# Kernel optimization log

Measured on AMD Instinct MI355X. Metric: run time of the kernel, lower is better.

Reference implementation:

```python
import jax, jax.numpy as jnp
import numpy as np

DIM = 256   # model dim (forced by gate Linear(32,4): d = 32 = DIM//H)
H = 8       # heads (hard-coded by mask.repeat(1,8,1,1))
D = DIM // H
B = 256     # batch
NS = 100    # skeleton tokens (sub-block size)
NQ = 64     # query tokens
N = NS + NQ # 164
NE = 4      # experts
HID = 50    # expert hidden
LN_EPS = 1e-5


def setup_inputs() -> dict:
    key = jax.random.key(0)
    ks = jax.random.split(key, 12)
    s = 0.02
    return {
        "x": jax.random.normal(ks[0], (B, N, DIM), jnp.float32),
        "mask": jax.random.randint(ks[1], (B, N), 0, 2).astype(bool),
        "w_qk_s": jax.random.normal(ks[2], (DIM, 2 * DIM), jnp.float32) * s,
        "w_qk_q": jax.random.normal(ks[3], (DIM, 2 * DIM), jnp.float32) * s,
        "w_v": jax.random.normal(ks[4], (DIM, DIM), jnp.float32) * s,
        "w_gate": jax.random.normal(ks[5], (D, NE), jnp.float32) * s,
        "b_gate": jnp.zeros((NE,), jnp.float32),
        "ln_gamma": jnp.ones((NE,), jnp.float32),
        "ln_beta": jnp.zeros((NE,), jnp.float32),
        "w1": jax.random.normal(ks[6], (NE, NS, HID), jnp.float32) * s,
        "b1": jnp.zeros((NE, HID), jnp.float32),
        "w2": jax.random.normal(ks[7], (NE, HID, NS), jnp.float32) * s,
        "b2": jnp.zeros((NE, NS), jnp.float32),
        "w_out": jax.random.normal(ks[8], (DIM, DIM), jnp.float32) * s,
        "b_out": jnp.zeros((DIM,), jnp.float32),
    }


def reference(x, mask, w_qk_s, w_qk_q, w_v, w_gate, b_gate, ln_gamma, ln_beta,
              w1, b1, w2, b2, w_out, b_out):
    b, n, dim = x.shape
    scale = dim ** -0.5  # scale_with_head=False -> dim**-0.5

    def to_heads(t):  # (b, m, H*D) -> (b, H, m, D)
        return t.reshape(b, -1, H, D).transpose(0, 2, 1, 3)

    # separate qk projections for skeleton (first 100) vs query (last 64) tokens
    q_s, k_s = jnp.split(x[:, :NS] @ w_qk_s, 2, axis=-1)
    q_q, k_q = jnp.split(x[:, NS:] @ w_qk_q, 2, axis=-1)
    q = jnp.concatenate([to_heads(q_s), to_heads(q_q)], axis=2)  # (b,H,N,D)
    k = jnp.concatenate([to_heads(k_s), to_heads(k_q)], axis=2)
    v = to_heads(x @ w_v)

    # gates: RAW reshape of x (b,n,H*D) -> (b,H,n,D) (memory reinterpretation,
    # as in torch x.reshape), detached, sliced to first 100 'rows'
    gx = jax.lax.stop_gradient(x).reshape(b, H, n, D)[:, :, :NS, :]
    g = gx @ w_gate + b_gate                              # (b,H,100,4)
    mu = g.mean(-1, keepdims=True)
    var = g.var(-1, keepdims=True)
    g = (g - mu) / jnp.sqrt(var + LN_EPS) * ln_gamma + ln_beta
    gates = jax.nn.softmax(g, axis=-1)                    # (b,H,100,4)

    dots = jnp.einsum('bhid,bhjd->bhij', q, k) * scale    # (b,H,N,N)
    mask_value = -jnp.finfo(dots.dtype).max
    dots = jnp.where(mask[:, None, None, :], mask_value, dots)

    # soft-MoE over the 100x100 sub-block (experts applied along key axis)
    attn_q = dots[:, :, :NS, :NS]                         # (b,H,100,100)
    h1 = jax.nn.relu(jnp.einsum('bhij,ejk->bheik', jax.nn.relu(attn_q), w1)
                     + b1[:, None, :])                    # (b,H,4,100,50)
    eo = jax.nn.relu(jnp.einsum('bheik,ekj->bheij', h1, w2)
                     + b2[:, None, :])                    # (b,H,4,100,100)
    moes = jnp.einsum('bheij,bhie->bhij', eo, gates)      # (b,H,100,100)

    dots = dots.at[:, :, :NS, :NS].add(moes)
    attn = jax.nn.softmax(dots, axis=-1)
    out = jnp.einsum('bhij,bhjd->bhid', attn, v)          # (b,H,N,D)
    out = out.transpose(0, 2, 1, 3).reshape(b, n, dim)
    return out @ w_out + b_out
```

## Files before the change

### kernel.cpp

```cpp
#include <hip/hip_runtime.h>

typedef __bf16 bf16x8 __attribute__((ext_vector_type(8)));
typedef __bf16 bf16x4 __attribute__((ext_vector_type(4)));
typedef float  f32x4  __attribute__((ext_vector_type(4)));

__device__ __forceinline__ bf16x8 ldb8(const __bf16* p) {
    return *reinterpret_cast<const bf16x8*>(p);
}
__device__ __forceinline__ bf16x8 zero8() {
    bf16x8 z;
    #pragma unroll
    for (int i = 0; i < 8; i++) z[i] = (__bf16)0.f;
    return z;
}
__device__ __forceinline__ __bf16 ldw(const void* p, int i, int m) {
    return m ? (__bf16)((const float*)p)[i] : ((const __bf16*)p)[i];
}
__device__ __forceinline__ bf16x8 ldx8(const void* p, size_t ei, int m) {
    if (m) {
        const float* f = (const float*)p + ei;
        f32x4 a = *reinterpret_cast<const f32x4*>(f);
        f32x4 b = *reinterpret_cast<const f32x4*>(f + 4);
        bf16x8 r;
        #pragma unroll
        for (int u = 0; u < 4; u++) { r[u] = (__bf16)a[u]; r[4 + u] = (__bf16)b[u]; }
        return r;
    }
    return ldb8((const __bf16*)p + ei);
}

__global__ __launch_bounds__(256) void detect_kernel(
    const void* x, const void* mask, int* modes, int* maskws)
{
    __shared__ int v32bad, v16bad, sbad;
    const int t = threadIdx.x, bid = blockIdx.x;
    if (t == 0) { v32bad = 0; v16bad = 0; sbad = 0; }
    __syncthreads();
    const unsigned int* mw = (const unsigned int*)mask;
    int b32 = 0, b16 = 0;
    for (int i = t; i < 10496; i += 256) {
        unsigned int w = mw[i];
        if (!(w == 0u || w == 1u || w == 0x3F800000u)) b32++;
        unsigned int h0 = w & 0xFFFFu, h1 = w >> 16;
        if (!(h0 == 0u || h0 == 1u || h0 == 0x3F80u)) b16++;
        if (!(h1 == 0u || h1 == 1u || h1 == 0x3F80u)) b16++;
    }
    if (b32) atomicAdd(&v32bad, b32);
    if (b16) atomicAdd(&v16bad, b16);
    if (bid == 0) {
        const unsigned int* xw = (const unsigned int*)x;
        int bad = 0;
        for (int i = t; i < 2048; i += 256) {
            unsigned int w = xw[i];
            unsigned int el = (w >> 7) & 0xFF, eh = (w >> 23) & 0xFF;
            if (el >= 0x94 || el == 0xFF) bad++;
            if (eh >= 0x94 || eh == 0xFF) bad++;
        }
        if (bad) atomicAdd(&sbad, bad);
    }
    __syncthreads();
    const int mmode = (v32bad == 0) ? 0 : ((v16bad == 0) ? 2 : 1);
    if (bid == 0 && t == 0) { modes[0] = (sbad > 64) ? 1 : 0; modes[1] = mmode; }
    const int lo = bid * 656, hi = lo + 656;
    for (int i = lo + t; i < hi; i += 256) {
        int val;
        if (mmode == 0)      val = (((const int*)mask)[i] != 0);
        else if (mmode == 2) val = (((const unsigned short*)mask)[i] != 0);
        else                 val = (((const unsigned char*)mask)[i] != 0);
        maskws[i] = val;
    }
}

__global__ __launch_bounds__(256) void prep_kernel(
    const void* wqks, const void* wqkq, const void* wv, const void* w1,
    const void* w2, const void* wout, const void* wg, const void* bg,
    const void* lng, const void* lnb, const void* b1, const void* b2,
    const void* bout, const int* __restrict__ modes,
    __bf16* __restrict__ Wts, __bf16* __restrict__ Wtq,
    __bf16* __restrict__ w1t, __bf16* __restrict__ w2t,
    __bf16* __restrict__ wot, __bf16* __restrict__ wsm)
{
    const int m = modes[0];
    int i = blockIdx.x * 256 + threadIdx.x;
    if (i < 196608) {
        int n = i >> 8, k = i & 255;
        __bf16 vs, vq;
        if (n < 512) { vs = ldw(wqks, k * 512 + n, m); vq = ldw(wqkq, k * 512 + n, m); }
        else         { vs = ldw(wv, k * 256 + (n - 512), m); vq = vs; }
        Wts[i] = vs; Wtq[i] = vq;
        return;
    }
    i -= 196608;
    if (i < 32768) {
        int e = i >> 13, r = i & 8191, n = r >> 7, k = r & 127;
        w1t[i] = (n < 50 && k < 100) ? ldw(w1, (e * 100 + k) * 50 + n, m) : (__bf16)0.f;
        return;
    }
    i -= 32768;
    if (i < 28672) {
        int e = i / 7168, r = i % 7168, n = r >> 6, k = r & 63;
        w2t[i] = (n < 100 && k < 50) ? ldw(w2, (e * 50 + k) * 100 + n, m) : (__bf16)0.f;
        return;
    }
    i -= 28672;
    if (i < 65536) {
        int n = i >> 8, k = i & 255;
        wot[i] = ldw(wout, k * 256 + n, m);
        return;
    }
    i -= 65536;
    if (i < 996) {
        __bf16 v;
        if (i < 128)      v = ldw(wg, i, m);
        else if (i < 132) v = ldw(bg, i - 128, m);
        else if (i < 136) v = ldw(lng, i - 132, m);
        else if (i < 140) v = ldw(lnb, i - 136, m);
        else if (i < 340) v = ldw(b1, i - 140, m);
        else if (i < 740) v = ldw(b2, i - 340, m);
        else              v = ldw(bout, i - 740, m);
        wsm[i] = v;
    }
}

__global__ __launch_bounds__(256, 2) void qkv_kernel(
    const void* __restrict__ x, const __bf16* __restrict__ Wts,
    const __bf16* __restrict__ Wtq, const __bf16* __restrict__ wsm,
    const int* __restrict__ modes,
    __bf16* __restrict__ q, __bf16* __restrict__ k, __bf16* __restrict__ vt,
    float* __restrict__ gates)
{
    __shared__ __bf16 xs[32][264];
    __shared__ float wgf[128];
    __shared__ float gcst[12];
    const int m = modes[0];
    const int b = blockIdx.y;
    const int mt = blockIdx.x >> 1;
    const int half = blockIdx.x & 1;
    const __bf16* Wt = (mt < 4) ? Wts : Wtq;
    const int rbase = (mt < 4) ? mt * 32 : 100 + (mt - 4) * 32;
    const int tid = threadIdx.x;

    if (tid < 128) wgf[tid] = (float)wsm[tid];
    if (tid < 12)  gcst[tid] = (float)wsm[128 + tid];
    for (int c = tid; c < 1024; c += 256) {
        int row = c >> 5, part = c & 31;
        bf16x8 val = ldx8(x, ((size_t)b * 164 + rbase + row) * 256 + part * 8, m);
        *reinterpret_cast<bf16x8*>(&xs[row][part * 8]) = val;
    }
    __syncthreads();

    if (half == 0) {
        int jg = rbase * 8 + tid;
        int h = jg / 164;
        int j = jg - h * 164;
        if (j < 100) {
            const __bf16* xp = &xs[tid >> 3][(tid & 7) * 32];
            float g[4] = {gcst[0], gcst[1], gcst[2], gcst[3]};
            #pragma unroll
            for (int p = 0; p < 4; p++) {
                bf16x8 xv = ldb8(xp + p * 8);
                #pragma unroll
                for (int u = 0; u < 8; u++) {
                    float f = (float)xv[u];
                    #pragma unroll
                    for (int e = 0; e < 4; e++) g[e] += f * wgf[(p * 8 + u) * 4 + e];
                }
            }
            float mu = 0.25f * (g[0] + g[1] + g[2] + g[3]);
            float var = 0.25f * ((g[0]-mu)*(g[0]-mu) + (g[1]-mu)*(g[1]-mu) +
                                 (g[2]-mu)*(g[2]-mu) + (g[3]-mu)*(g[3]-mu));
            float is = rsqrtf(var + 1e-5f);
            float mx = -3.0e38f;
            #pragma unroll
            for (int e = 0; e < 4; e++) {
                g[e] = (g[e] - mu) * is * gcst[4 + e] + gcst[8 + e];
                mx = fmaxf(mx, g[e]);
            }
            float s = 0.f;
            #pragma unroll
            for (int e = 0; e < 4; e++) { g[e] = __expf(g[e] - mx); s += g[e]; }
            float inv = 1.f / s;
            float4 gv = make_float4(g[0]*inv, g[1]*inv, g[2]*inv, g[3]*inv);
            *reinterpret_cast<float4*>(&gates[((size_t)(b * 8 + h) * 100 + j) * 4]) = gv;
        }
    }

    const int w = tid >> 6, l = tid & 63, lr = l & 15, lc = l >> 4;
    f32x4 acc[2][6];
    #pragma unroll
    for (int ms = 0; ms < 2; ms++)
        #pragma unroll
        for (int nt = 0; nt < 6; nt++) acc[ms][nt] = (f32x4){0.f, 0.f, 0.f, 0.f};

    #pragma unroll
    for (int kt = 0; kt < 8; kt++) {
        bf16x8 a0 = ldb8(&xs[lr][kt * 32 + lc * 8]);
        bf16x8 a1 = ldb8(&xs[16 + lr][kt * 32 + lc * 8]);
        #pragma unroll
        for (int nt = 0; nt < 6; nt++) {
            bf16x8 bb = ldb8(Wt + (size_t)(half * 384 + w * 96 + nt * 16 + lr) * 256 + kt * 32 + lc * 8);
            acc[0][nt] = __builtin_amdgcn_mfma_f32_16x16x32_bf16(a0, bb, acc[0][nt], 0, 0, 0);
            acc[1][nt] = __builtin_amdgcn_mfma_f32_16x16x32_bf16(a1, bb, acc[1][nt], 0, 0, 0);
        }
    }
    #pragma unroll
    for (int ms = 0; ms < 2; ms++) {
        #pragma unroll
        for (int nt = 0; nt < 6; nt++) {
            int c = half * 384 + w * 96 + nt * 16 + lr;
            int i0 = rbase + ms * 16 + lc * 4;
            if (c < 512) {
                __bf16* dst; int ch;
                if (c < 256) { dst = q; ch = c; }
                else         { dst = k; ch = c - 256; }
                int hh = ch >> 5, d = ch & 31;
                #pragma unroll
                for (int r = 0; r < 4; r++) {
                    int i = i0 + r;
                    if (mt >= 4 || i < 100)
                        dst[(((size_t)b * 8 + hh) * 164 + i) * 32 + d] = (__bf16)acc[ms][nt][r];
                }
            } else {
                int ch = c - 512, hh = ch >> 5, d = ch & 31;
                if (mt >= 4 || i0 < 100) {
                    bf16x4 pv;
                    #pragma unroll
                    for (int r = 0; r < 4; r++) pv[r] = (__bf16)acc[ms][nt][r];
                    *reinterpret_cast<bf16x4*>(&vt[((size_t)(b * 8 + hh) * 32 + d) * 176 + i0]) = pv;
                }
            }
        }
    }
}

__global__ __launch_bounds__(256, 4) void attn_kernel(
    const __bf16* __restrict__ qg, const __bf16* __restrict__ kg,
    const __bf16* __restrict__ vtg, const float* __restrict__ gatesg,
    const int* __restrict__ maskg, const __bf16* __restrict__ w1t,
    const __bf16* __restrict__ w2t, const __bf16* __restrict__ wsm,
    __bf16* __restrict__ ohg)
{
    __shared__ __align__(16) __bf16 lds[20352];
    const int RS_OFF = 7040;
    const int P_OFF  = 7040;

    const __bf16* b1g = wsm + 140;
    const __bf16* b2g = wsm + 340;
    const int bh = blockIdx.x, rt = blockIdx.y, b = bh >> 3, tid = threadIdx.x;
    const int w = tid >> 6, l = tid & 63, lr = l & 15, lc = l >> 4;
    const int m0 = w * 16;

    const __bf16* kbase = kg + (size_t)bh * 164 * 32;
    for (int c = tid; c < 704; c += 256) {
        int row = c >> 2, part = c & 3;
        bf16x8 val = (row < 164) ? ldb8(kbase + row * 32 + part * 8) : zero8();
        *reinterpret_cast<bf16x8*>(&lds[row * 40 + part * 8]) = val;
    }
    unsigned mbits = 0;
    #pragma unroll
    for (int nt = 0; nt < 11; nt++) {
        int j = nt * 16 + lr;
        int bad = (j < 164) ? maskg[b * 164 + j] : 1;
        mbits |= (bad ? 1u : 0u) << nt;
    }
    int qrow = rt * 64 + m0 + lr; if (qrow > 163) qrow = 163;
    bf16x8 afq = ldb8(qg + ((size_t)bh * 164 + qrow) * 32 + lc * 8);
    __syncthreads();

    f32x4 raw[12];
    #pragma unroll
    for (int nt = 0; nt < 11; nt++) {
        bf16x8 bf = ldb8(&lds[(nt * 16 + lr) * 40 + lc * 8]);
        f32x4 acc = {0.f, 0.f, 0.f, 0.f};
        acc = __builtin_amdgcn_mfma_f32_16x16x32_bf16(afq, bf, acc, 0, 0, 0);
        bool bad = (mbits >> nt) & 1;
        #pragma unroll
        for (int r = 0; r < 4; r++)
            raw[nt][r] = bad ? -1e30f : acc[r] * 0.0625f;
    }
    #pragma unroll
    for (int r = 0; r < 4; r++) raw[11][r] = -1e30f;

    if (rt < 2) {
        #pragma unroll
        for (int nt = 0; nt < 8; nt++) {
            int j = nt * 16 + lr;
            #pragma unroll
            for (int r = 0; r < 4; r++) {
                float v = raw[nt][r];
                v = (j >= 100 || v < 0.f) ? 0.f : v;
                lds[RS_OFF + (m0 + lc * 4 + r) * 136 + j] = (__bf16)v;
            }
        }
    }
    __syncthreads();

    if (rt < 2) {
        const int gi0 = rt * 64 + m0 + lc * 4;
        float4 gv[4];
        #pragma unroll
        for (int r = 0; r < 4; r++) {
            int gi = gi0 + r;
            gv[r] = (gi < 100)
                ? *reinterpret_cast<const float4*>(&gatesg[((size_t)bh * 100 + gi) * 4])
                : make_float4(0.f, 0.f, 0.f, 0.f);
        }
        bf16x8 sa[4];
        #pragma unroll
        for (int kt = 0; kt < 4; kt++)
            sa[kt] = ldb8(&lds[RS_OFF + (m0 + lr) * 136 + kt * 32 + lc * 8]);
        #pragma unroll
        for (int e = 0; e < 4; e++) {
            const int HO = (e & 1) ? 15744 : 0;
            #pragma unroll
            for (int nt = 0; nt < 4; nt++) {
                f32x4 acc = {0.f, 0.f, 0.f, 0.f};
                #pragma unroll
                for (int kt = 0; kt < 4; kt++) {
                    bf16x8 bb = ldb8(w1t + (size_t)(e * 64 + nt * 16 + lr) * 128 + kt * 32 + lc * 8);
                    acc = __builtin_amdgcn_mfma_f32_16x16x32_bf16(sa[kt], bb, acc, 0, 0, 0);
                }
                int n = nt * 16 + lr;
                float bias = (n < 50) ? (float)b1g[e * 50 + n] : 0.f;
                #pragma unroll
                for (int r = 0; r < 4; r++) {
                    float v = acc[r] + bias;
                    if (v < 0.f) v = 0.f;
                    lds[HO + (m0 + lc * 4 + r) * 72 + n] = (__bf16)v;
                }
            }
            bf16x8 ha0 = ldb8(&lds[HO + (m0 + lr) * 72 + lc * 8]);
            bf16x8 ha1 = ldb8(&lds[HO + (m0 + lr) * 72 + 32 + lc * 8]);
            #pragma unroll
            for (int nt = 0; nt < 7; nt++) {
                f32x4 acc = {0.f, 0.f, 0.f, 0.f};
                bf16x8 bb0 = ldb8(w2t + (size_t)(e * 112 + nt * 16 + lr) * 64 + lc * 8);
                acc = __builtin_amdgcn_mfma_f32_16x16x32_bf16(ha0, bb0, acc, 0, 0, 0);
                bf16x8 bb1 = ldb8(w2t + (size_t)(e * 112 + nt * 16 + lr) * 64 + 32 + lc * 8);
                acc = __builtin_amdgcn_mfma_f32_16x16x32_bf16(ha1, bb1, acc, 0, 0, 0);
                int n = nt * 16 + lr;
                float bias = (n < 100) ? (float)b2g[e * 100 + n] : 0.f;
                #pragma unroll
                for (int r = 0; r < 4; r++) {
                    float v = acc[r] + bias;
                    if (v < 0.f) v = 0.f;
                    float ge = (e == 0) ? gv[r].x : (e == 1) ? gv[r].y
                             : (e == 2) ? gv[r].z : gv[r].w;
                    raw[nt][r] += v * ge;
                }
            }
        }
    }
    __syncthreads();

    const __bf16* vtb = vtg + (size_t)bh * 32 * 176;
    int off0, off1, off2;
    bf16x8 vv0, vv1, vv2;
    {
        int c = tid;
        int row = c / 22, j0 = (c - row * 22) * 8;
        off0 = row * 200 + j0;
        if (j0 < 168) {
            vv0 = ldb8(vtb + row * 176 + j0);
            if (j0 == 160) { vv0[4] = (__bf16)0.f; vv0[5] = (__bf16)0.f; vv0[6] = (__bf16)0.f; vv0[7] = (__bf16)0.f; }
        } else vv0 = zero8();
    }
    {
        int c = tid + 256;
        int row = c / 22, j0 = (c - row * 22) * 8;
        off1 = row * 200 + j0;
        if (j0 < 168) {
            vv1 = ldb8(vtb + row * 176 + j0);
            if (j0 == 160) { vv1[4] = (__bf16)0.f; vv1[5] = (__bf16)0.f; vv1[6] = (__bf16)0.f; vv1[7] = (__bf16)0.f; }
        } else vv1 = zero8();
    }
    if (tid < 192) {
        int c = tid + 512;
        int row = c / 22, j0 = (c - row * 22) * 8;
        off2 = row * 200 + j0;
        if (j0 < 168) {
            vv2 = ldb8(vtb + row * 176 + j0);
            if (j0 == 160) { vv2[4] = (__bf16)0.f; vv2[5] = (__bf16)0.f; vv2[6] = (__bf16)0.f; vv2[7] = (__bf16)0.f; }
        } else vv2 = zero8();
    }

    #pragma unroll
    for (int r = 0; r < 4; r++) {
        float x0 = fmaxf(raw[0][r], raw[1][r]);
        float x1 = fmaxf(raw[2][r], raw[3][r]);
        float x2 = fmaxf(raw[4][r], raw[5][r]);
        float x3 = fmaxf(raw[6][r], raw[7][r]);
        float x4 = fmaxf(raw[8][r], raw[9][r]);
        float x5 = fmaxf(raw[10][r], raw[11][r]);
        float m2 = fmaxf(fmaxf(fmaxf(x0, x1), fmaxf(x2, x3)), fmaxf(x4, x5));
        m2 = fmaxf(m2, __shfl_xor(m2, 1, 64));
        m2 = fmaxf(m2, __shfl_xor(m2, 2, 64));
        m2 = fmaxf(m2, __shfl_xor(m2, 4, 64));
        m2 = fmaxf(m2, __shfl_xor(m2, 8, 64));
        #pragma unroll
        for (int nt = 0; nt < 12; nt++) raw[nt][r] = __expf(raw[nt][r] - m2);
        float s0 = (raw[0][r] + raw[1][r]) + (raw[2][r] + raw[3][r]);
        float s1 = (raw[4][r] + raw[5][r]) + (raw[6][r] + raw[7][r]);
        float s2t = (raw[8][r] + raw[9][r]) + (raw[10][r] + raw[11][r]);
        float s2 = (s0 + s1) + s2t;
        s2 += __shfl_xor(s2, 1, 64);
        s2 += __shfl_xor(s2, 2, 64);
        s2 += __shfl_xor(s2, 4, 64);
        s2 += __shfl_xor(s2, 8, 64);
        float inv = (s2 > 0.f) ? 1.f / s2 : 0.f;
        #pragma unroll
        for (int nt = 0; nt < 12; nt++)
            lds[P_OFF + (m0 + lc * 4 + r) * 200 + nt * 16 + lr] = (__bf16)(raw[nt][r] * inv);
    }

    *reinterpret_cast<bf16x8*>(&lds[off0]) = vv0;
    *reinterpret_cast<bf16x8*>(&lds[off1]) = vv1;
    if (tid < 192) *reinterpret_cast<bf16x8*>(&lds[off2]) = vv2;
    __syncthreads();

    int gi = rt * 64 + m0 + lr;
    #pragma unroll
    for (int nt = 0; nt < 2; nt++) {
        f32x4 acc = {0.f, 0.f, 0.f, 0.f};
        #pragma unroll
        for (int kt = 0; kt < 6; kt++) {
            bf16x8 va = ldb8(&lds[(nt * 16 + lr) * 200 + kt * 32 + lc * 8]);
            bf16x8 pb = ldb8(&lds[P_OFF + (m0 + lr) * 200 + kt * 32 + lc * 8]);
            acc = __builtin_amdgcn_mfma_f32_16x16x32_bf16(va, pb, acc, 0, 0, 0);
        }
        if (gi < 164) {
            bf16x4 ov;
            #pragma unroll
            for (int r = 0; r < 4; r++) ov[r] = (__bf16)acc[r];
            *reinterpret_cast<bf16x4*>(&ohg[((size_t)bh * 164 + gi) * 32 + nt * 16 + lc * 4]) = ov;
        }
    }
}

__global__ __launch_bounds__(256) void outproj_kernel(
    const __bf16* __restrict__ oh, const __bf16* __restrict__ wot,
    const __bf16* __restrict__ wsm, float* __restrict__ out)
{
    const __bf16* bout = wsm + 740;
    const int b = blockIdx.y;
    const int mt = blockIdx.x >> 2;
    const int ntile = blockIdx.x & 3;
    const int tid = threadIdx.x;
    const int w = tid >> 6, l = tid & 63, lr = l & 15, lc = l >> 4;
    int row = mt * 64 + w * 16 + lr; if (row > 163) row = 163;
    f32x4 acc[4];
    #pragma unroll
    for (int nt = 0; nt < 4; nt++) acc[nt] = (f32x4){0.f, 0.f, 0.f, 0.f};
    #pragma unroll
    for (int kt = 0; kt < 8; kt++) {
        bf16x8 a = ldb8(oh + (((size_t)b * 8 + kt) * 164 + row) * 32 + lc * 8);
        #pragma unroll
        for (int nt = 0; nt < 4; nt++) {
            bf16x8 bb = ldb8(wot + (size_t)(ntile * 64 + nt * 16 + lr) * 256 + kt * 32 + lc * 8);
            acc[nt] = __builtin_amdgcn_mfma_f32_16x16x32_bf16(a, bb, acc[nt], 0, 0, 0);
        }
    }
    #pragma unroll
    for (int nt = 0; nt < 4; nt++) {
        int n = ntile * 64 + nt * 16 + lr;
        float bias = (float)bout[n];
        #pragma unroll
        for (int r = 0; r < 4; r++) {
            int i = mt * 64 + w * 16 + lc * 4 + r;
            if (i < 164)
                out[((size_t)b * 164 + i) * 256 + n] = acc[nt][r] + bias;
        }
    }
}

extern "C" void kernel_launch(void* const* d_in, const int* in_sizes, int n_in,
                              void* d_out, int out_size, void* d_ws, size_t ws_size,
                              hipStream_t stream) {
    const void* x      = d_in[0];
    const void* mask   = d_in[1];
    const void* w_qk_s = d_in[2];
    const void* w_qk_q = d_in[3];
    const void* w_v    = d_in[4];
    const void* w_gate = d_in[5];
    const void* b_gate = d_in[6];
    const void* ln_g   = d_in[7];
    const void* ln_b   = d_in[8];
    const void* w1     = d_in[9];
    const void* b1     = d_in[10];
    const void* w2     = d_in[11];
    const void* b2     = d_in[12];
    const void* w_out  = d_in[13];
    const void* b_out  = d_in[14];
    float* out = (float*)d_out;

    char* ws = (char*)d_ws;
    size_t off = 0;
    auto nextp = [&](size_t bytes) {
        char* p = ws + off;
        off += (bytes + 255) & ~(size_t)255;
        return p;
    };
    const size_t QKV_ELEMS = (size_t)256 * 8 * 164 * 32;
    const size_t VT_ELEMS  = (size_t)256 * 8 * 32 * 176;
    int*    modes  = (int*)nextp(64);
    int*    maskws = (int*)nextp((size_t)41984 * 4);
    __bf16* qws  = (__bf16*)nextp(QKV_ELEMS * 2);
    __bf16* kws  = (__bf16*)nextp(QKV_ELEMS * 2);
    __bf16* vtws = (__bf16*)nextp(VT_ELEMS * 2);
    __bf16* ohws = (__bf16*)nextp(QKV_ELEMS * 2);
    float*  gws  = (float*)nextp((size_t)2048 * 100 * 4 * 4);
    __bf16* Wts  = (__bf16*)nextp(768 * 256 * 2);
    __bf16* Wtq  = (__bf16*)nextp(768 * 256 * 2);
    __bf16* w1t  = (__bf16*)nextp(4 * 64 * 128 * 2);
    __bf16* w2t  = (__bf16*)nextp(4 * 112 * 64 * 2);
    __bf16* wot  = (__bf16*)nextp(256 * 256 * 2);
    __bf16* wsm  = (__bf16*)nextp(996 * 2);

    detect_kernel<<<64, 256, 0, stream>>>(x, mask, modes, maskws);
    prep_kernel<<<1268, 256, 0, stream>>>(w_qk_s, w_qk_q, w_v, w1, w2, w_out,
                                          w_gate, b_gate, ln_g, ln_b, b1, b2,
                                          b_out, modes, Wts, Wtq, w1t, w2t, wot, wsm);
    qkv_kernel<<<dim3(12, 256), 256, 0, stream>>>(x, Wts, Wtq, wsm, modes,
                                                  qws, kws, vtws, gws);
    attn_kernel<<<dim3(2048, 3), 256, 0, stream>>>(qws, kws, vtws, gws, maskws,
                                                   w1t, w2t, wsm, ohws);
    outproj_kernel<<<dim3(12, 256), 256, 0, stream>>>(ohws, wot, wsm, out);
}
```

Measured before the change: 592.8 us.

## Cut register pressure in attention kernel and move V staging before MoE

Drops the padding score tile, so 11 score fragments stay in registers instead of 12, and explicitly zeroes the last P column block. The MoE loop over experts is no longer unrolled. Gate values are now loaded per expert as scalars instead of held in float4 registers, and the skeleton-score A fragments are reloaded per expert. The V transpose staging into LDS moves ahead of the MoE phase into a region the MoE phase does not use, and MFMA sections are wrapped in s_setprio. The aim is to lower VGPR use for the 4-waves occupancy target and avoid spills, at the cost of extra LDS and global reloads and a single shared h1 buffer.

```diff
diff --git a/kernel.cpp b/kernel.cpp
--- a/kernel.cpp
+++ b/kernel.cpp
@@ -243,6 +243,7 @@
     __shared__ __align__(16) __bf16 lds[20352];
     const int RS_OFF = 7040;
     const int P_OFF  = 7040;
+    const int H1_OFF = 15744;
 
     const __bf16* b1g = wsm + 140;
     const __bf16* b2g = wsm + 340;
@@ -267,7 +268,8 @@
     bf16x8 afq = ldb8(qg + ((size_t)bh * 164 + qrow) * 32 + lc * 8);
     __syncthreads();
 
-    f32x4 raw[12];
+    f32x4 raw[11];
+    __builtin_amdgcn_s_setprio(1);
     #pragma unroll
     for (int nt = 0; nt < 11; nt++) {
         bf16x8 bf = ldb8(&lds[(nt * 16 + lr) * 40 + lc * 8]);
@@ -278,8 +280,7 @@
         for (int r = 0; r < 4; r++)
             raw[nt][r] = bad ? -1e30f : acc[r] * 0.0625f;
     }
-    #pragma unroll
-    for (int r = 0; r < 4; r++) raw[11][r] = -1e30f;
+    __builtin_amdgcn_s_setprio(0);
 
     if (rt < 2) {
         #pragma unroll
@@ -295,139 +296,115 @@
     }
     __syncthreads();
 
+    const __bf16* vtb = vtg + (size_t)bh * 32 * 176;
+    #pragma unroll
+    for (int p = 0; p < 3; p++) {
+        int c = tid + p * 256;
+        int row = c / 24, jc = c - row * 24, j0 = jc * 8;
+        bf16x8 vv;
+        if (j0 < 164) {
+            vv = ldb8(vtb + row * 176 + j0);
+            if (j0 == 160) { vv[4] = (__bf16)0.f; vv[5] = (__bf16)0.f; vv[6] = (__bf16)0.f; vv[7] = (__bf16)0.f; }
+        } else vv = zero8();
+        *reinterpret_cast<bf16x8*>(&lds[row * 200 + j0]) = vv;
+    }
+
     if (rt < 2) {
         const int gi0 = rt * 64 + m0 + lc * 4;
-        float4 gv[4];
-        #pragma unroll
-        for (int r = 0; r < 4; r++) {
-            int gi = gi0 + r;
-            gv[r] = (gi < 100)
-                ? *reinterpret_cast<const float4*>(&gatesg[((size_t)bh * 100 + gi) * 4])
-                : make_float4(0.f, 0.f, 0.f, 0.f);
-        }
-        bf16x8 sa[4];
-        #pragma unroll
-        for (int kt = 0; kt < 4; kt++)
-            sa[kt] = ldb8(&lds[RS_OFF + (m0 + lr) * 136 + kt * 32 + lc * 8]);
-        #pragma unroll
         for (int e = 0; e < 4; e++) {
-            const int HO = (e & 1) ? 15744 : 0;
+            bf16x8 sa[4];
+            #pragma unroll
+            for (int kt = 0; kt < 4; kt++)
+                sa[kt] = ldb8(&lds[RS_OFF + (m0 + lr) * 136 + kt * 32 + lc * 8]);
             #pragma unroll
             for (int nt = 0; nt < 4; nt++) {
                 f32x4 acc = {0.f, 0.f, 0.f, 0.f};
+                __builtin_amdgcn_s_setprio(1);
                 #pragma unroll
                 for (int kt = 0; kt < 4; kt++) {
                     bf16x8 bb = ldb8(w1t + (size_t)(e * 64 + nt * 16 + lr) * 128 + kt * 32 + lc * 8);
                     acc = __builtin_amdgcn_mfma_f32_16x16x32_bf16(sa[kt], bb, acc, 0, 0, 0);
                 }
+                __builtin_amdgcn_s_setprio(0);
                 int n = nt * 16 + lr;
                 float bias = (n < 50) ? (float)b1g[e * 50 + n] : 0.f;
                 #pragma unroll
                 for (int r = 0; r < 4; r++) {
                     float v = acc[r] + bias;
                     if (v < 0.f) v = 0.f;
-                    lds[HO + (m0 + lc * 4 + r) * 72 + n] = (__bf16)v;
+                    lds[H1_OFF + (m0 + lc * 4 + r) * 72 + n] = (__bf16)v;
                 }
             }
-            bf16x8 ha0 = ldb8(&lds[HO + (m0 + lr) * 72 + lc * 8]);
-            bf16x8 ha1 = ldb8(&lds[HO + (m0 + lr) * 72 + 32 + lc * 8]);
+            bf16x8 ha0 = ldb8(&lds[H1_OFF + (m0 + lr) * 72 + lc * 8]);
+            bf16x8 ha1 = ldb8(&lds[H1_OFF + (m0 + lr) * 72 + 32 + lc * 8]);
+            float gt[4];
+            #pragma unroll
+            for (int r = 0; r < 4; r++) {
+                int gi = gi0 + r;
+                gt[r] = (gi < 100) ? gatesg[((size_t)bh * 100 + gi) * 4 + e] : 0.f;
+            }
             #pragma unroll
             for (int nt = 0; nt < 7; nt++) {
                 f32x4 acc = {0.f, 0.f, 0.f, 0.f};
+                __builtin_amdgcn_s_setprio(1);
                 bf16x8 bb0 = ldb8(w2t + (size_t)(e * 112 + nt * 16 + lr) * 64 + lc * 8);
                 acc = __builtin_amdgcn_mfma_f32_16x16x32_bf16(ha0, bb0, acc, 0, 0, 0);
                 bf16x8 bb1 = ldb8(w2t + (size_t)(e * 112 + nt * 16 + lr) * 64 + 32 + lc * 8);
                 acc = __builtin_amdgcn_mfma_f32_16x16x32_bf16(ha1, bb1, acc, 0, 0, 0);
+                __builtin_amdgcn_s_setprio(0);
                 int n = nt * 16 + lr;
                 float bias = (n < 100) ? (float)b2g[e * 100 + n] : 0.f;
                 #pragma unroll
                 for (int r = 0; r < 4; r++) {
                     float v = acc[r] + bias;
                     if (v < 0.f) v = 0.f;
-                    float ge = (e == 0) ? gv[r].x : (e == 1) ? gv[r].y
-                             : (e == 2) ? gv[r].z : gv[r].w;
-                    raw[nt][r] += v * ge;
+                    raw[nt][r] += v * gt[r];
                 }
             }
         }
     }
     __syncthreads();
 
-    const __bf16* vtb = vtg + (size_t)bh * 32 * 176;
-    int off0, off1, off2;
-    bf16x8 vv0, vv1, vv2;
-    {
-        int c = tid;
-        int row = c / 22, j0 = (c - row * 22) * 8;
-        off0 = row * 200 + j0;
-        if (j0 < 168) {
-            vv0 = ldb8(vtb + row * 176 + j0);
-            if (j0 == 160) { vv0[4] = (__bf16)0.f; vv0[5] = (__bf16)0.f; vv0[6] = (__bf16)0.f; vv0[7] = (__bf16)0.f; }
-        } else vv0 = zero8();
-    }
-    {
-        int c = tid + 256;
-        int row = c / 22, j0 = (c - row * 22) * 8;
-        off1 = row * 200 + j0;
-        if (j0 < 168) {
-            vv1 = ldb8(vtb + row * 176 + j0);
-            if (j0 == 160) { vv1[4] = (__bf16)0.f; vv1[5] = (__bf16)0.f; vv1[6] = (__bf16)0.f; vv1[7] = (__bf16)0.f; }
-        } else vv1 = zero8();
-    }
-    if (tid < 192) {
-        int c = tid + 512;
-        int row = c / 22, j0 = (c - row * 22) * 8;
-        off2 = row * 200 + j0;
-        if (j0 < 168) {
-            vv2 = ldb8(vtb + row * 176 + j0);
-            if (j0 == 160) { vv2[4] = (__bf16)0.f; vv2[5] = (__bf16)0.f; vv2[6] = (__bf16)0.f; vv2[7] = (__bf16)0.f; }
-        } else vv2 = zero8();
-    }
-
     #pragma unroll
     for (int r = 0; r < 4; r++) {
-        float x0 = fmaxf(raw[0][r], raw[1][r]);
-        float x1 = fmaxf(raw[2][r], raw[3][r]);
-        float x2 = fmaxf(raw[4][r], raw[5][r]);
-        float x3 = fmaxf(raw[6][r], raw[7][r]);
-        float x4 = fmaxf(raw[8][r], raw[9][r]);
-        float x5 = fmaxf(raw[10][r], raw[11][r]);
-        float m2 = fmaxf(fmaxf(fmaxf(x0, x1), fmaxf(x2, x3)), fmaxf(x4, x5));
+        float m2 = raw[0][r];
+        #pragma unroll
+        for (int nt = 1; nt < 11; nt++) m2 = fmaxf(m2, raw[nt][r]);
         m2 = fmaxf(m2, __shfl_xor(m2, 1, 64));
         m2 = fmaxf(m2, __shfl_xor(m2, 2, 64));
         m2 = fmaxf(m2, __shfl_xor(m2, 4, 64));
         m2 = fmaxf(m2, __shfl_xor(m2, 8, 64));
-        #pragma unroll
-        for (int nt = 0; nt < 12; nt++) raw[nt][r] = __expf(raw[nt][r] - m2);
-        float s0 = (raw[0][r] + raw[1][r]) + (raw[2][r] + raw[3][r]);
-        float s1 = (raw[4][r] + raw[5][r]) + (raw[6][r] + raw[7][r]);
-        float s2t = (raw[8][r] + raw[9][r]) + (raw[10][r] + raw[11][r]);
-        float s2 = (s0 + s1) + s2t;
+        float s2 = 0.f;
+        #pragma unroll
+        for (int nt = 0; nt < 11; nt++) {
+            float ev = __expf(raw[nt][r] - m2);
+            raw[nt][r] = ev;
+            s2 += ev;
+        }
         s2 += __shfl_xor(s2, 1, 64);
         s2 += __shfl_xor(s2, 2, 64);
         s2 += __shfl_xor(s2, 4, 64);
         s2 += __shfl_xor(s2, 8, 64);
         float inv = (s2 > 0.f) ? 1.f / s2 : 0.f;
         #pragma unroll
-        for (int nt = 0; nt < 12; nt++)
+        for (int nt = 0; nt < 11; nt++)
             lds[P_OFF + (m0 + lc * 4 + r) * 200 + nt * 16 + lr] = (__bf16)(raw[nt][r] * inv);
-    }
-
-    *reinterpret_cast<bf16x8*>(&lds[off0]) = vv0;
-    *reinterpret_cast<bf16x8*>(&lds[off1]) = vv1;
-    if (tid < 192) *reinterpret_cast<bf16x8*>(&lds[off2]) = vv2;
+        lds[P_OFF + (m0 + lc * 4 + r) * 200 + 176 + lr] = (__bf16)0.f;
+    }
     __syncthreads();
 
     int gi = rt * 64 + m0 + lr;
     #pragma unroll
     for (int nt = 0; nt < 2; nt++) {
         f32x4 acc = {0.f, 0.f, 0.f, 0.f};
+        __builtin_amdgcn_s_setprio(1);
         #pragma unroll
         for (int kt = 0; kt < 6; kt++) {
             bf16x8 va = ldb8(&lds[(nt * 16 + lr) * 200 + kt * 32 + lc * 8]);
             bf16x8 pb = ldb8(&lds[P_OFF + (m0 + lr) * 200 + kt * 32 + lc * 8]);
             acc = __builtin_amdgcn_mfma_f32_16x16x32_bf16(va, pb, acc, 0, 0, 0);
         }
+        __builtin_amdgcn_s_setprio(0);
         if (gi < 164) {
             bf16x4 ov;
             #pragma unroll
```

Result: faster. 520.0 us (-12.3%).
